# Performance work log

Measured on AMD Instinct MI355X. Metric: run time of the kernel, lower is better.

## Reference

```python
import jax, jax.numpy as jnp
import numpy as np

POINT_NB = 256
DILATION = 1
EPS = 1e-4  # pad mask value used by shiftFeat (0.0001)


def _shift(where, f, d):
    """Replicate-pad shift of f:[B,C,H,W]; returns shifted features and
    channel-averaged validity mask [B,1,H,W] (1 inside, EPS in pad region)."""
    B, C, H, W = f.shape
    m = jnp.ones((B, 1, H, W), dtype=f.dtype)
    if where == 'none':
        return f, m
    if where == 'left':
        fs = jnp.concatenate([f[..., d:], jnp.broadcast_to(f[..., -1:], (B, C, H, d))], axis=-1)
        m = m.at[..., -d:].set(EPS)
    elif where == 'right':
        fs = jnp.concatenate([jnp.broadcast_to(f[..., :1], (B, C, H, d)), f[..., :-d]], axis=-1)
        m = m.at[..., :d].set(EPS)
    elif where == 'top':
        fs = jnp.concatenate([f[:, :, d:, :], jnp.broadcast_to(f[:, :, -1:, :], (B, C, d, W))], axis=2)
        m = m.at[:, :, -d:, :].set(EPS)
    elif where == 'bot':
        fs = jnp.concatenate([jnp.broadcast_to(f[:, :, :1, :], (B, C, d, W)), f[:, :, :-d, :]], axis=2)
        m = m.at[:, :, :d, :].set(EPS)
    else:
        raise ValueError(where)
    return fs, m


def _cos_sim(f1, f2, m1, m2):
    # sim = sum(f1*f2*m1*m2, C) / (||m1*f1|| * ||m2*f2||); masks are [B,1,H,W], m>0
    num = (m1 * m2) * jnp.sum(f1 * f2, axis=1, keepdims=True)
    den = (m1 * jnp.sqrt(jnp.sum(f1 * f1, axis=1, keepdims=True))) * \
          (m2 * jnp.sqrt(jnp.sum(f2 * f2, axis=1, keepdims=True)))
    return num / den


def _total_sim(features, d):
    f1, m1 = _shift('right', features, d)
    f2, m2 = _shift('left', features, d)
    horiz = _cos_sim(f1, f2, m1, m2)
    f1, m1 = _shift('top', features, d)
    f2, m2 = _shift('bot', features, d)
    verti = _cos_sim(f1, f2, m1, m2)
    return (horiz + verti) * 0.5  # [B,1,H,W]


def setup_inputs() -> dict:
    key = jax.random.key(0)
    features = jax.random.normal(key, (16, 256, 56, 56), dtype=jnp.float32)
    return {"features": features}


def reference(features):
    B, C, H, W = features.shape
    sim = _total_sim(features, DILATION)            # [B,1,H,W]
    flat = sim.reshape(B, H * W)                    # [B,HW]
    vals, idx = jax.lax.top_k(flat, POINT_NB)       # [B,K]
    ycoord = idx // W
    xcoord = idx % W
    # gather feature vectors at selected points: [B,C,HW] -> [B,K,C]
    feat_flat = features.reshape(B, C, H * W)
    point_feat = jnp.take_along_axis(feat_flat, idx[:, None, :], axis=2)
    point_feat = jnp.transpose(point_feat, (0, 2, 1))
    return point_feat, vals, ycoord, xcoord
```

## Files before the change

### kernel.cpp

```cpp
#include <hip/hip_runtime.h>

#define NB 16
#define NC 256
#define NH 56
#define NW 56
#define NHW (NH * NW)
#define NK 256
#define CAP 1024

#define BR 8
#define RS 10
#define CS 8
#define CQ 64
#define NCHUNK (CQ / CS)
#define CHUNK16 (CS * RS * NW / 4)
#define NBAND (NH / BR)
#define P1_BLOCKS (NB * NBAND * 4)
#define NQ (BR * (NW / 4))
#define MAPS (NB * NHW)

__device__ inline unsigned int flip_f32(float f) {
    unsigned int u = __float_as_uint(f);
    return (u & 0x80000000u) ? ~u : (u | 0x80000000u);
}
__device__ inline float unflip_f32(unsigned int u) {
    u = (u & 0x80000000u) ? (u ^ 0x80000000u) : ~u;
    return __uint_as_float(u);
}

__global__ void __launch_bounds__(256)
pass1_kernel(const float* __restrict__ f, float* __restrict__ maps) {
    __shared__ __align__(16) float buf[2][CS * RS * NW];
    __shared__ float redbuf[NQ][2][12];

    int bid = blockIdx.x;
    int sb = (bid & 7) * (P1_BLOCKS / 8) + (bid >> 3);
    int b = sb / 28;
    int rem0 = sb - b * 28;
    int band = rem0 >> 2;
    int chq = rem0 & 3;
    int y0 = band * BR;
    int tid = threadIdx.x;
    const float* fb = f + (size_t)b * NC * NHW + (size_t)chq * CQ * NHW;

    auto stage = [&](int ci, float* dst) {
        int c0 = ci * CS;
#pragma unroll
        for (int i = 0; i < 5; ++i) {
            int k = tid + 256 * i;
            if (k < CHUNK16) {
                int ch = k / (RS * 14);
                int rem = k - ch * (RS * 14);
                int rl = rem / 14;
                int xk = rem - rl * 14;
                int rg = y0 - 1 + rl;
                rg = rg < 0 ? 0 : (rg > NH - 1 ? NH - 1 : rg);
                const float* src = fb + (size_t)(c0 + ch) * NHW + rg * NW + xk * 4;
                __builtin_amdgcn_global_load_lds(
                    (const __attribute__((address_space(1))) void*)src,
                    (__attribute__((address_space(3))) void*)(dst + k * 4),
                    16, 0, 0);
            }
        }
    };

    int chg = tid / NQ;
    int quad = tid - chg * NQ;
    int r = quad / 14, qx = quad - r * 14, x0 = qx * 4;
    int xl = x0 ? x0 - 1 : 0;
    int xr = (x0 + 4 < NW) ? x0 + 4 : NW - 1;

    float n0 = 0.f, n1 = 0.f, n2 = 0.f, n3 = 0.f;
    float h0 = 0.f, h1 = 0.f, h2 = 0.f, h3 = 0.f;
    float w0 = 0.f, w1 = 0.f, w2 = 0.f, w3 = 0.f;

    stage(0, buf[0]);
    __syncthreads();
    for (int ci = 0; ci < NCHUNK; ++ci) {
        if (ci + 1 < NCHUNK) stage(ci + 1, buf[(ci + 1) & 1]);
        if (tid < 2 * NQ) {
            const float* sbf = buf[ci & 1];
#pragma unroll
            for (int c = 0; c < 4; ++c) {
                const float* Bm = sbf + (chg * 4 + c) * (RS * NW) + (r + 1) * NW;
                float4 v = *(const float4*)(Bm + x0);
                float  l = Bm[xl];
                float  rr = Bm[xr];
                float4 u = *(const float4*)(Bm + NW + x0);
                float4 d = *(const float4*)(Bm - NW + x0);
                n0 += v.x * v.x; n1 += v.y * v.y; n2 += v.z * v.z; n3 += v.w * v.w;
                h0 += l * v.y;   h1 += v.x * v.z; h2 += v.y * v.w; h3 += v.z * rr;
                w0 += u.x * d.x; w1 += u.y * d.y; w2 += u.z * d.z; w3 += u.w * d.w;
            }
        }
        __syncthreads();
    }

    if (tid < 2 * NQ) {
        float* rb = redbuf[quad][chg];
        rb[0] = n0; rb[1] = n1; rb[2]  = n2; rb[3]  = n3;
        rb[4] = h0; rb[5] = h1; rb[6]  = h2; rb[7]  = h3;
        rb[8] = w0; rb[9] = w1; rb[10] = w2; rb[11] = w3;
    }
    __syncthreads();

    float* mbase = maps + (size_t)chq * 3 * MAPS;
    for (int oi = tid; oi < NQ * 12; oi += 256) {
        int q = oi / 12, comp = oi - q * 12;
        float acc = redbuf[q][0][comp] + redbuf[q][1][comp];
        int r2 = q / 14, qx2 = q - r2 * 14;
        int j = comp & 3;
        float* m = mbase + (size_t)(comp >> 2) * MAPS;
        m[((size_t)b * NH + y0 + r2) * NW + qx2 * 4 + j] = acc;
    }
}

__global__ void __launch_bounds__(256)
sim_kernel(const float* __restrict__ maps, unsigned int* __restrict__ sv) {
    int pix = blockIdx.x * 256 + threadIdx.x;
    if (pix >= NB * NHW) return;
    int b = pix / NHW, i = pix - b * NHW;

    int y = i / NW, x = i - y * NW;
    int xl = (x > 0) ? x - 1 : 0;
    int xr = (x < NW - 1) ? x + 1 : NW - 1;
    int yu = (y < NH - 1) ? y + 1 : NH - 1;
    int yd = (y > 0) ? y - 1 : 0;
    int il = y * NW + xl, ir = y * NW + xr;
    int iu = yu * NW + x, id = yd * NW + x;

    float nl = 0.f, nr = 0.f, nu = 0.f, nd = 0.f, h = 0.f, v = 0.f;
#pragma unroll
    for (int q = 0; q < 4; ++q) {
        const float* nq = maps + (size_t)(q * 3 + 0) * MAPS + (size_t)b * NHW;
        const float* hq = maps + (size_t)(q * 3 + 1) * MAPS + (size_t)b * NHW;
        const float* vq = maps + (size_t)(q * 3 + 2) * MAPS + (size_t)b * NHW;
        nl += nq[il]; nr += nq[ir]; nu += nq[iu]; nd += nq[id];
        h  += hq[i];  v  += vq[i];
    }
    float s = 0.5f * (h / (sqrtf(nl) * sqrtf(nr)) + v / (sqrtf(nu) * sqrtf(nd)));
    sv[pix] = flip_f32(s);
}

__global__ void __launch_bounds__(1024)
topk_kernel(const unsigned int* __restrict__ sv, int* __restrict__ idx_out,
            float* __restrict__ vals_out, float* __restrict__ y_out,
            float* __restrict__ x_out) {
    __shared__ unsigned int svals[NHW];
    __shared__ unsigned int hist[4096];
    __shared__ unsigned int wtot[16];
    __shared__ unsigned long long cand[CAP];
    __shared__ unsigned int sh_prefix, sh_mask;
    __shared__ int sh_above, sh_setS, sh_done, sh_cnt;

    const int b = blockIdx.x;
    const int tid = threadIdx.x;
    const int lane = tid & 63;
    const int wv = tid >> 6;
    const unsigned int* svb = sv + (size_t)b * NHW;

    for (int i = tid; i < NHW; i += 1024) svals[i] = svb[i];
    if (tid == 0) { sh_prefix = 0u; sh_mask = 0u; sh_above = 0; sh_done = 0; }

    const int shifts[3] = {20, 8, 0};
    const unsigned int wmasks[3] = {0xFFFu, 0xFFFu, 0xFFu};
    for (int st = 0; st < 3; ++st) {
        __syncthreads();
        int kneed = NK - sh_above;
        if (sh_done) break;
        for (int i = tid; i < 4096; i += 1024) hist[i] = 0u;
        __syncthreads();
        unsigned int pfx = sh_prefix, msk = sh_mask;
        int shift = shifts[st];
        unsigned int wmask = wmasks[st];
        for (int i = tid; i < NHW; i += 1024) {
            unsigned int v = svals[i];
            if ((v & msk) == pfx) atomicAdd(&hist[(v >> shift) & wmask], 1u);
        }
        __syncthreads();
        unsigned int b0 = hist[4 * tid], b1 = hist[4 * tid + 1];
        unsigned int b2 = hist[4 * tid + 2], b3 = hist[4 * tid + 3];
        unsigned int lsum = b0 + b1 + b2 + b3;
        unsigned int s = lsum;
#pragma unroll
        for (int d = 1; d < 64; d <<= 1) {
            unsigned int t2 = __shfl_down(s, d);
            s += (lane + d < 64) ? t2 : 0u;
        }
        if (lane == 0) wtot[wv] = s;
        __syncthreads();
        unsigned int wabove = 0;
        for (int w = wv + 1; w < 16; ++w) wabove += wtot[w];
        unsigned int thr_above = wabove + (s - lsum);
        unsigned int suf3 = thr_above + b3;
        unsigned int suf2 = suf3 + b2;
        unsigned int suf1 = suf2 + b1;
        unsigned int suf0 = suf1 + b0;
        if (suf0 >= (unsigned int)kneed && thr_above < (unsigned int)kneed) {
            int c; unsigned int above, hc;
            if (suf3 >= (unsigned int)kneed)      { c = 4 * tid + 3; above = thr_above; hc = b3; }
            else if (suf2 >= (unsigned int)kneed) { c = 4 * tid + 2; above = suf3;      hc = b2; }
            else if (suf1 >= (unsigned int)kneed) { c = 4 * tid + 1; above = suf2;      hc = b1; }
            else                                  { c = 4 * tid + 0; above = suf1;      hc = b0; }
            sh_above += (int)above;
            sh_setS = (int)hc;
            sh_prefix = pfx | ((unsigned int)c << shift);
            sh_mask = msk | (wmask << shift);
            if (sh_above + sh_setS <= CAP || st == 2) sh_done = 1;
        }
    }
    __syncthreads();

    if (tid == 0) sh_cnt = 0;
    __syncthreads();
    unsigned int T = sh_prefix;
    for (int i = tid; i < NHW; i += 1024) {
        unsigned int v = svals[i];
        bool keep = (v >= T);
        unsigned long long m = __ballot(keep);
        int basep = 0;
        if (lane == 0) basep = atomicAdd(&sh_cnt, __popcll(m));
        basep = __shfl(basep, 0);
        if (keep) {
            int pos = basep + __popcll(m & ((1ull << lane) - 1ull));
            if (pos < CAP)
                cand[pos] = ((unsigned long long)v << 32) |
                            (unsigned long long)(0xFFFFFFFFu - (unsigned int)i);
        }
    }
    __syncthreads();
    int nc = sh_cnt; if (nc > CAP) nc = CAP;

    if (tid < nc) {
        unsigned long long my = cand[tid];
        int rank = 0;
        for (int i = 0; i < nc; ++i) rank += (cand[i] > my);
        if (rank < NK) {
            unsigned int lo = (unsigned int)(my & 0xFFFFFFFFull);
            int idx = (int)(0xFFFFFFFFu - lo);
            float val = unflip_f32((unsigned int)(my >> 32));
            int o = b * NK + rank;
            idx_out[o] = idx;
            vals_out[o] = val;
            y_out[o] = (float)(idx / NW);
            x_out[o] = (float)(idx % NW);
        }
    }
}

#define GCT 8
__global__ void __launch_bounds__(256)
gather_kernel(const float* __restrict__ f, const int* __restrict__ idx,
              float* __restrict__ out) {
    int bid = blockIdx.x;
    int b = bid >> 5;
    int c0 = (bid & 31) * GCT;
    int t = threadIdx.x;
    int p = idx[b * NK + t];
    const float* fb = f + (size_t)b * NC * NHW + (size_t)c0 * NHW;

    float v[GCT];
#pragma unroll
    for (int ci = 0; ci < GCT; ++ci) v[ci] = fb[(size_t)ci * NHW + p];

    float4 a = make_float4(v[0], v[1], v[2], v[3]);
    float4 b4 = make_float4(v[4], v[5], v[6], v[7]);
    float* op = out + ((size_t)b * NK + t) * NC + c0;
    *(float4*)op = a;
    *(float4*)(op + 4) = b4;
}

extern "C" void kernel_launch(void* const* d_in, const int* in_sizes, int n_in,
                              void* d_out, int out_size, void* d_ws, size_t ws_size,
                              hipStream_t stream) {
    const float* f = (const float*)d_in[0];

    float* out_feat = (float*)d_out;
    float* out_vals = out_feat + (size_t)NB * NK * NC;
    float* out_y    = out_vals + (size_t)NB * NK;
    float* out_x    = out_y    + (size_t)NB * NK;

    float* maps = (float*)d_ws;
    unsigned int* sv = (unsigned int*)(maps + 12 * (size_t)MAPS);
    int* idx = (int*)(sv + MAPS);

    pass1_kernel<<<P1_BLOCKS, 256, 0, stream>>>(f, maps);
    sim_kernel<<<(NB * NHW + 255) / 256, 256, 0, stream>>>(maps, sv);
    topk_kernel<<<NB, 1024, 0, stream>>>(sv, idx, out_vals, out_y, out_x);
    gather_kernel<<<NB * (NC / GCT), 256, 0, stream>>>(f, idx, out_feat);
}
```

Measured before the change: 37.72 us.

## Build first-level top-k histogram in sim kernel via per-slice byte histograms

The sim kernel now computes per-slice 4096-bin histograms of the top 12 bits of the similarity keys and writes them as packed byte counts. The top-k kernel sums these 14 slice histograms instead of running its first histogram pass, and it reads similarity values straight from global memory instead of staging them in shared memory. This moves the first radix pass out of the single-block-per-batch top-k kernel, which has low parallelism. In exchange it adds extra global traffic for the slices, adds re-reads of sv from global memory in the later passes, and relies on byte counters not overflowing, which holds because each slice has only 224 pixels.

```diff
diff --git a/kernel.cpp b/kernel.cpp
--- a/kernel.cpp
+++ b/kernel.cpp
@@ -18,6 +18,10 @@
 #define P1_BLOCKS (NB * NBAND * 4)
 #define NQ (BR * (NW / 4))
 #define MAPS (NB * NHW)
+
+#define SPB 14
+#define SPX 224
+#define NBIN 4096
 
 __device__ inline unsigned int flip_f32(float f) {
     unsigned int u = __float_as_uint(f);
@@ -116,38 +120,61 @@
 }
 
 __global__ void __launch_bounds__(256)
-sim_kernel(const float* __restrict__ maps, unsigned int* __restrict__ sv) {
-    int pix = blockIdx.x * 256 + threadIdx.x;
-    if (pix >= NB * NHW) return;
-    int b = pix / NHW, i = pix - b * NHW;
-
-    int y = i / NW, x = i - y * NW;
-    int xl = (x > 0) ? x - 1 : 0;
-    int xr = (x < NW - 1) ? x + 1 : NW - 1;
-    int yu = (y < NH - 1) ? y + 1 : NH - 1;
-    int yd = (y > 0) ? y - 1 : 0;
-    int il = y * NW + xl, ir = y * NW + xr;
-    int iu = yu * NW + x, id = yd * NW + x;
-
-    float nl = 0.f, nr = 0.f, nu = 0.f, nd = 0.f, h = 0.f, v = 0.f;
-#pragma unroll
-    for (int q = 0; q < 4; ++q) {
-        const float* nq = maps + (size_t)(q * 3 + 0) * MAPS + (size_t)b * NHW;
-        const float* hq = maps + (size_t)(q * 3 + 1) * MAPS + (size_t)b * NHW;
-        const float* vq = maps + (size_t)(q * 3 + 2) * MAPS + (size_t)b * NHW;
-        nl += nq[il]; nr += nq[ir]; nu += nq[iu]; nd += nq[id];
-        h  += hq[i];  v  += vq[i];
-    }
-    float s = 0.5f * (h / (sqrtf(nl) * sqrtf(nr)) + v / (sqrtf(nu) * sqrtf(nd)));
-    sv[pix] = flip_f32(s);
+sim_kernel(const float* __restrict__ maps, unsigned int* __restrict__ sv,
+           unsigned char* __restrict__ slices) {
+    __shared__ unsigned int hist[NBIN];
+
+    int bid = blockIdx.x;
+    int b = bid / SPB;
+    int sl = bid - b * SPB;
+    int tid = threadIdx.x;
+
+    for (int j = tid; j < NBIN; j += 256) hist[j] = 0u;
+    __syncthreads();
+
+    if (tid < SPX) {
+        int i = sl * SPX + tid;
+        int pix = b * NHW + i;
+        int y = i / NW, x = i - y * NW;
+        int xl = (x > 0) ? x - 1 : 0;
+        int xr = (x < NW - 1) ? x + 1 : NW - 1;
+        int yu = (y < NH - 1) ? y + 1 : NH - 1;
+        int yd = (y > 0) ? y - 1 : 0;
+        int il = y * NW + xl, ir = y * NW + xr;
+        int iu = yu * NW + x, id = yd * NW + x;
+
+        float nl = 0.f, nr = 0.f, nu = 0.f, nd = 0.f, h = 0.f, v = 0.f;
+#pragma unroll
+        for (int q = 0; q < 4; ++q) {
+            const float* nq = maps + (size_t)(q * 3 + 0) * MAPS + (size_t)b * NHW;
+            const float* hq = maps + (size_t)(q * 3 + 1) * MAPS + (size_t)b * NHW;
+            const float* vq = maps + (size_t)(q * 3 + 2) * MAPS + (size_t)b * NHW;
+            nl += nq[il]; nr += nq[ir]; nu += nq[iu]; nd += nq[id];
+            h  += hq[i];  v  += vq[i];
+        }
+        float s = 0.5f * (h / (sqrtf(nl) * sqrtf(nr)) + v / (sqrtf(nu) * sqrtf(nd)));
+        unsigned int fv = flip_f32(s);
+        sv[pix] = fv;
+        atomicAdd(&hist[fv >> 20], 1u);
+    }
+    __syncthreads();
+
+    unsigned char* out = slices + (size_t)bid * NBIN;
+    for (int j = tid; j < NBIN / 4; j += 256) {
+        unsigned int h4 = (hist[4 * j + 0] & 0xFFu)
+                        | ((hist[4 * j + 1] & 0xFFu) << 8)
+                        | ((hist[4 * j + 2] & 0xFFu) << 16)
+                        | ((hist[4 * j + 3] & 0xFFu) << 24);
+        ((unsigned int*)out)[j] = h4;
+    }
 }
 
 __global__ void __launch_bounds__(1024)
-topk_kernel(const unsigned int* __restrict__ sv, int* __restrict__ idx_out,
-            float* __restrict__ vals_out, float* __restrict__ y_out,
-            float* __restrict__ x_out) {
-    __shared__ unsigned int svals[NHW];
-    __shared__ unsigned int hist[4096];
+topk_kernel(const unsigned int* __restrict__ sv,
+            const unsigned char* __restrict__ slices,
+            int* __restrict__ idx_out, float* __restrict__ vals_out,
+            float* __restrict__ y_out, float* __restrict__ x_out) {
+    __shared__ unsigned int hist[NBIN];
     __shared__ unsigned int wtot[16];
     __shared__ unsigned long long cand[CAP];
     __shared__ unsigned int sh_prefix, sh_mask;
@@ -159,27 +186,23 @@
     const int wv = tid >> 6;
     const unsigned int* svb = sv + (size_t)b * NHW;
 
-    for (int i = tid; i < NHW; i += 1024) svals[i] = svb[i];
     if (tid == 0) { sh_prefix = 0u; sh_mask = 0u; sh_above = 0; sh_done = 0; }
 
-    const int shifts[3] = {20, 8, 0};
-    const unsigned int wmasks[3] = {0xFFFu, 0xFFFu, 0xFFu};
-    for (int st = 0; st < 3; ++st) {
-        __syncthreads();
-        int kneed = NK - sh_above;
-        if (sh_done) break;
-        for (int i = tid; i < 4096; i += 1024) hist[i] = 0u;
-        __syncthreads();
-        unsigned int pfx = sh_prefix, msk = sh_mask;
-        int shift = shifts[st];
-        unsigned int wmask = wmasks[st];
-        for (int i = tid; i < NHW; i += 1024) {
-            unsigned int v = svals[i];
-            if ((v & msk) == pfx) atomicAdd(&hist[(v >> shift) & wmask], 1u);
-        }
-        __syncthreads();
-        unsigned int b0 = hist[4 * tid], b1 = hist[4 * tid + 1];
-        unsigned int b2 = hist[4 * tid + 2], b3 = hist[4 * tid + 3];
+    unsigned int b0 = 0, b1 = 0, b2 = 0, b3 = 0;
+    {
+        const unsigned int* slb = (const unsigned int*)(slices + (size_t)b * SPB * NBIN);
+#pragma unroll
+        for (int s = 0; s < SPB; ++s) {
+            unsigned int q = slb[s * (NBIN / 4) + tid];
+            b0 += q & 0xFFu;
+            b1 += (q >> 8) & 0xFFu;
+            b2 += (q >> 16) & 0xFFu;
+            b3 += (q >> 24) & 0xFFu;
+        }
+    }
+    __syncthreads();
+    {
+        const unsigned int kneed = NK;
         unsigned int lsum = b0 + b1 + b2 + b3;
         unsigned int s = lsum;
 #pragma unroll
@@ -196,17 +219,65 @@
         unsigned int suf2 = suf3 + b2;
         unsigned int suf1 = suf2 + b1;
         unsigned int suf0 = suf1 + b0;
+        if (suf0 >= kneed && thr_above < kneed) {
+            int c; unsigned int above, hc;
+            if (suf3 >= kneed)      { c = 4 * tid + 3; above = thr_above; hc = b3; }
+            else if (suf2 >= kneed) { c = 4 * tid + 2; above = suf3;      hc = b2; }
+            else if (suf1 >= kneed) { c = 4 * tid + 1; above = suf2;      hc = b1; }
+            else                    { c = 4 * tid + 0; above = suf1;      hc = b0; }
+            sh_above = (int)above;
+            sh_setS = (int)hc;
+            sh_prefix = ((unsigned int)c) << 20;
+            sh_mask = 0xFFFu << 20;
+            if ((int)above + (int)hc <= CAP) sh_done = 1;
+        }
+    }
+
+    const int shifts[2] = {8, 0};
+    const unsigned int wmasks[2] = {0xFFFu, 0xFFu};
+    for (int st = 0; st < 2; ++st) {
+        __syncthreads();
+        int kneed = NK - sh_above;
+        if (sh_done) break;
+        for (int i = tid; i < NBIN; i += 1024) hist[i] = 0u;
+        __syncthreads();
+        unsigned int pfx = sh_prefix, msk = sh_mask;
+        int shift = shifts[st];
+        unsigned int wmask = wmasks[st];
+        for (int i = tid; i < NHW; i += 1024) {
+            unsigned int v = svb[i];
+            if ((v & msk) == pfx) atomicAdd(&hist[(v >> shift) & wmask], 1u);
+        }
+        __syncthreads();
+        unsigned int c0 = hist[4 * tid], c1 = hist[4 * tid + 1];
+        unsigned int c2 = hist[4 * tid + 2], c3 = hist[4 * tid + 3];
+        unsigned int lsum = c0 + c1 + c2 + c3;
+        unsigned int s = lsum;
+#pragma unroll
+        for (int d = 1; d < 64; d <<= 1) {
+            unsigned int t2 = __shfl_down(s, d);
+            s += (lane + d < 64) ? t2 : 0u;
+        }
+        if (lane == 0) wtot[wv] = s;
+        __syncthreads();
+        unsigned int wabove = 0;
+        for (int w = wv + 1; w < 16; ++w) wabove += wtot[w];
+        unsigned int thr_above = wabove + (s - lsum);
+        unsigned int suf3 = thr_above + c3;
+        unsigned int suf2 = suf3 + c2;
+        unsigned int suf1 = suf2 + c1;
+        unsigned int suf0 = suf1 + c0;
         if (suf0 >= (unsigned int)kneed && thr_above < (unsigned int)kneed) {
             int c; unsigned int above, hc;
-            if (suf3 >= (unsigned int)kneed)      { c = 4 * tid + 3; above = thr_above; hc = b3; }
-            else if (suf2 >= (unsigned int)kneed) { c = 4 * tid + 2; above = suf3;      hc = b2; }
-            else if (suf1 >= (unsigned int)kneed) { c = 4 * tid + 1; above = suf2;      hc = b1; }
-            else                                  { c = 4 * tid + 0; above = suf1;      hc = b0; }
+            if (suf3 >= (unsigned int)kneed)      { c = 4 * tid + 3; above = thr_above; hc = c3; }
+            else if (suf2 >= (unsigned int)kneed) { c = 4 * tid + 2; above = suf3;      hc = c2; }
+            else if (suf1 >= (unsigned int)kneed) { c = 4 * tid + 1; above = suf2;      hc = c1; }
+            else                                  { c = 4 * tid + 0; above = suf1;      hc = c0; }
             sh_above += (int)above;
             sh_setS = (int)hc;
             sh_prefix = pfx | ((unsigned int)c << shift);
             sh_mask = msk | (wmask << shift);
-            if (sh_above + sh_setS <= CAP || st == 2) sh_done = 1;
+            if (sh_above + sh_setS <= CAP || st == 1) sh_done = 1;
         }
     }
     __syncthreads();
@@ -215,7 +286,7 @@
     __syncthreads();
     unsigned int T = sh_prefix;
     for (int i = tid; i < NHW; i += 1024) {
-        unsigned int v = svals[i];
+        unsigned int v = svb[i];
         bool keep = (v >= T);
         unsigned long long m = __ballot(keep);
         int basep = 0;
@@ -282,10 +353,11 @@
 
     float* maps = (float*)d_ws;
     unsigned int* sv = (unsigned int*)(maps + 12 * (size_t)MAPS);
-    int* idx = (int*)(sv + MAPS);
+    unsigned char* slices = (unsigned char*)(sv + MAPS);
+    int* idx = (int*)(slices + (size_t)NB * SPB * NBIN);
 
     pass1_kernel<<<P1_BLOCKS, 256, 0, stream>>>(f, maps);
-    sim_kernel<<<(NB * NHW + 255) / 256, 256, 0, stream>>>(maps, sv);
-    topk_kernel<<<NB, 1024, 0, stream>>>(sv, idx, out_vals, out_y, out_x);
+    sim_kernel<<<NB * SPB, 256, 0, stream>>>(maps, sv, slices);
+    topk_kernel<<<NB, 1024, 0, stream>>>(sv, slices, idx, out_vals, out_y, out_x);
     gather_kernel<<<NB * (NC / GCT), 256, 0, stream>>>(f, idx, out_feat);
 }
```

Result: no change. 38.45 us (+1.9%).
